# Optimization experiments

Measured on AMD Instinct MI355X. Metric: run time of the kernel, lower is better.

## Reference

```python
import jax, jax.numpy as jnp
import numpy as np

N_TOKENS = 1 << 20   # free dim; all feature dims hardcoded in the module
D_IN, D_MODEL, D_OUT = 4, 16, 4
N_EXPERTS = 8


def setup_inputs() -> dict:
    key = jax.random.key(0)
    ks = jax.random.split(key, 12)
    s = 1.0 / np.sqrt(D_MODEL)
    return {
        "x":        jax.random.normal(ks[0], (N_TOKENS, D_IN), jnp.float32),
        "w_embed":  jax.random.normal(ks[1], (D_IN, D_MODEL), jnp.float32) * 0.5,
        "b_embed":  jax.random.normal(ks[2], (D_MODEL,), jnp.float32) * 0.1,
        "gate_w":   jax.random.normal(ks[3], (D_MODEL, N_EXPERTS), jnp.float32) * s,
        "expert_w": jax.random.normal(ks[4], (N_EXPERTS, D_MODEL, D_MODEL), jnp.float32) * s,
        "expert_b": jax.random.normal(ks[5], (N_EXPERTS, D_MODEL), jnp.float32) * 0.1,
        "resid_w":  jax.random.normal(ks[6], (D_MODEL, D_MODEL), jnp.float32) * s,
        "resid_b":  jax.random.normal(ks[7], (D_MODEL,), jnp.float32) * 0.1,
        "comb_w":   jax.random.normal(ks[8], (D_MODEL, 2), jnp.float32) * s,
        "comb_b":   jax.random.normal(ks[9], (2,), jnp.float32) * 0.1,
        "proj_w":   jax.random.normal(ks[10], (D_MODEL, D_OUT), jnp.float32) * s,
        "proj_b":   jax.random.normal(ks[11], (D_OUT,), jnp.float32) * 0.1,
    }


def reference(x, w_embed, b_embed, gate_w, expert_w, expert_b,
              resid_w, resid_b, comb_w, comb_b, proj_w, proj_b):
    # embed: Linear(4, 16)
    h = x @ w_embed + b_embed                       # [N, 16]

    # top-1 softmax router (residual MoE forces top_k = 1)
    gates = jax.nn.softmax(h @ gate_w, axis=-1)     # [N, E]
    idx = jnp.argmax(gates, axis=-1)                # [N] int, constant wrt grads
    onehot = jax.nn.one_hot(idx, N_EXPERTS, dtype=h.dtype)  # [N, E]

    # load-balancing aux loss: E * sum(mean_prob * mean_dispatch)
    aux = N_EXPERTS * jnp.sum(gates.mean(0) * onehot.mean(0))

    # expert dispatch + combine (dense-equivalent of gather/scatter)
    exp_out = jnp.einsum('nd,edh->enh', h, expert_w) + expert_b[:, None, :]  # [E, N, 16]
    moe_out = jnp.einsum('ne,enh->nh', onehot, exp_out)                      # [N, 16]
    gate_sel = jnp.sum(gates * onehot, axis=-1, keepdims=True)               # [N, 1]
    moe_out = moe_out * gate_sel

    # residual expert + learned combine weights
    resid = h @ resid_w + resid_b                   # [N, 16]
    cw = jax.nn.softmax(h @ comb_w + comb_b, -1)    # [N, 2]
    y = moe_out * cw[:, :1] + resid * cw[:, 1:2]

    # proj: Linear(16, 4); aux loss is accumulated in MOE_CONTEXT in the original
    out = y @ proj_w + proj_b                       # [N, 4]
    return out, aux
```

## Files before the change

kernel.cpp:

```cpp
#include <hip/hip_runtime.h>

#define NSLOTS 128

__global__ __launch_bounds__(256) void moe_main(
    const float* __restrict__ xg,
    const float* __restrict__ w_embed,
    const float* __restrict__ b_embed,
    const float* __restrict__ gate_w,
    const float* __restrict__ expert_w,
    const float* __restrict__ expert_b,
    const float* __restrict__ resid_w,
    const float* __restrict__ resid_b,
    const float* __restrict__ comb_w,
    const float* __restrict__ comb_b,
    const float* __restrict__ proj_w,
    const float* __restrict__ proj_b,
    float* __restrict__ out,
    float* __restrict__ ws,
    int ntok)
{
    __shared__ float EP[8][16][4];
    __shared__ float RP[16][4];
    __shared__ __align__(16) float tblE[8][20];
    __shared__ __align__(16) float tblR[20];
    __shared__ __align__(16) float tblC[12];

    const int tid = threadIdx.x;

    #pragma unroll
    for (int r = 0; r < 2; ++r) {
        int idx = tid + 256 * r;
        int e = idx >> 6, rem = idx & 63, d = rem >> 2, j = rem & 3;
        float s = 0.0f;
        #pragma unroll
        for (int h = 0; h < 16; ++h)
            s = fmaf(expert_w[e * 256 + d * 16 + h], proj_w[h * 4 + j], s);
        EP[e][d][j] = s;
    }
    if (tid < 64) {
        int d = tid >> 2, j = tid & 3;
        float s = 0.0f;
        #pragma unroll
        for (int h = 0; h < 16; ++h)
            s = fmaf(resid_w[d * 16 + h], proj_w[h * 4 + j], s);
        RP[d][j] = s;
    }
    __syncthreads();

    if (tid < 128) {
        int e = tid >> 4, i = (tid >> 2) & 3, j = tid & 3;
        float s = 0.0f;
        #pragma unroll
        for (int d = 0; d < 16; ++d) s = fmaf(w_embed[i * 16 + d], EP[e][d][j], s);
        tblE[e][i * 4 + j] = s;
    } else if (tid < 160) {
        int q = tid - 128, e = q >> 2, j = q & 3;
        float s = 0.0f;
        #pragma unroll
        for (int d = 0; d < 16; ++d) s = fmaf(b_embed[d], EP[e][d][j], s);
        #pragma unroll
        for (int h = 0; h < 16; ++h) s = fmaf(expert_b[e * 16 + h], proj_w[h * 4 + j], s);
        tblE[e][16 + j] = s;
    } else if (tid < 176) {
        int q = tid - 160, i = q >> 2, j = q & 3;
        float s = 0.0f;
        #pragma unroll
        for (int d = 0; d < 16; ++d) s = fmaf(w_embed[i * 16 + d], RP[d][j], s);
        tblR[i * 4 + j] = s;
    } else if (tid < 180) {
        int j = tid - 176;
        float s = 0.0f;
        #pragma unroll
        for (int d = 0; d < 16; ++d) s = fmaf(b_embed[d], RP[d][j], s);
        #pragma unroll
        for (int h = 0; h < 16; ++h) s = fmaf(resid_b[h], proj_w[h * 4 + j], s);
        tblR[16 + j] = s;
    } else if (tid < 188) {
        int q = tid - 180, i = q >> 1, c = q & 1;
        float s = 0.0f;
        #pragma unroll
        for (int d = 0; d < 16; ++d) s = fmaf(w_embed[i * 16 + d], comb_w[d * 2 + c], s);
        tblC[i * 2 + c] = s;
    } else if (tid < 190) {
        int c = tid - 188;
        float s = comb_b[c];
        #pragma unroll
        for (int d = 0; d < 16; ++d) s = fmaf(b_embed[d], comb_w[d * 2 + c], s);
        tblC[8 + c] = s;
    }
    __syncthreads();

    float rpx[16], cr[4], cwx[8], cc[2];
    #pragma unroll
    for (int i = 0; i < 16; ++i) rpx[i] = tblR[i];
    #pragma unroll
    for (int j = 0; j < 4; ++j) cr[j] = tblR[16 + j];
    #pragma unroll
    for (int i = 0; i < 8; ++i) cwx[i] = tblC[i];
    cc[0] = tblC[8]; cc[1] = tblC[9];

    float psum[8], pcnt[8];
    #pragma unroll
    for (int e = 0; e < 8; ++e) { psum[e] = 0.0f; pcnt[e] = 0.0f; }

    #pragma unroll
    for (int t = 0; t < 2; ++t) {
        int nid = blockIdx.x * 512 + t * 256 + tid;
        if (nid < ntok) {
            float4 xv = ((const float4*)xg)[nid];

            float h[16];
            #pragma unroll
            for (int k = 0; k < 16; ++k) {
                float s = xv.x * w_embed[k];
                s = fmaf(xv.y, w_embed[16 + k], s);
                s = fmaf(xv.z, w_embed[32 + k], s);
                s = fmaf(xv.w, w_embed[48 + k], s);
                h[k] = s + b_embed[k];
            }

            float lg[8];
            #pragma unroll
            for (int e = 0; e < 8; ++e) {
                float s = h[0] * gate_w[e];
                #pragma unroll
                for (int k = 1; k < 16; ++k) s = fmaf(h[k], gate_w[k * 8 + e], s);
                lg[e] = s;
            }
            float m = lg[0]; int sel = 0;
            #pragma unroll
            for (int e = 1; e < 8; ++e) { if (lg[e] > m) { m = lg[e]; sel = e; } }
            float p[8], S = 0.0f;
            #pragma unroll
            for (int e = 0; e < 8; ++e) { p[e] = __expf(lg[e] - m); S += p[e]; }
            float inv = 1.0f / S;
            #pragma unroll
            for (int e = 0; e < 8; ++e) psum[e] = fmaf(p[e], inv, psum[e]);
            #pragma unroll
            for (int e = 0; e < 8; ++e) pcnt[e] += (sel == e) ? 1.0f : 0.0f;
            float gs = inv;

            const float4* tep = (const float4*)(&tblE[sel][0]);
            float te[20];
            #pragma unroll
            for (int q = 0; q < 5; ++q) {
                float4 v = tep[q];
                te[4 * q + 0] = v.x; te[4 * q + 1] = v.y;
                te[4 * q + 2] = v.z; te[4 * q + 3] = v.w;
            }

            float mo[4], rp[4];
            #pragma unroll
            for (int j = 0; j < 4; ++j) {
                float s = te[16 + j];
                s = fmaf(xv.x, te[j],      s);
                s = fmaf(xv.y, te[4 + j],  s);
                s = fmaf(xv.z, te[8 + j],  s);
                s = fmaf(xv.w, te[12 + j], s);
                mo[j] = s;
                float r = cr[j];
                r = fmaf(xv.x, rpx[j],      r);
                r = fmaf(xv.y, rpx[4 + j],  r);
                r = fmaf(xv.z, rpx[8 + j],  r);
                r = fmaf(xv.w, rpx[12 + j], r);
                rp[j] = r;
            }

            float l0 = cc[0], l1 = cc[1];
            l0 = fmaf(xv.x, cwx[0], l0); l1 = fmaf(xv.x, cwx[1], l1);
            l0 = fmaf(xv.y, cwx[2], l0); l1 = fmaf(xv.y, cwx[3], l1);
            l0 = fmaf(xv.z, cwx[4], l0); l1 = fmaf(xv.z, cwx[5], l1);
            l0 = fmaf(xv.w, cwx[6], l0); l1 = fmaf(xv.w, cwx[7], l1);
            float cm = fmaxf(l0, l1);
            float t0 = __expf(l0 - cm), t1 = __expf(l1 - cm);
            float ci = 1.0f / (t0 + t1);
            float cw0 = t0 * ci, cw1 = t1 * ci;

            float a = gs * cw0;
            float4 ov;
            ov.x = fmaf(a, mo[0], fmaf(cw1, rp[0], proj_b[0]));
            ov.y = fmaf(a, mo[1], fmaf(cw1, rp[1], proj_b[1]));
            ov.z = fmaf(a, mo[2], fmaf(cw1, rp[2], proj_b[2]));
            ov.w = fmaf(a, mo[3], fmaf(cw1, rp[3], proj_b[3]));
            ((float4*)out)[nid] = ov;
        }
    }

    {
        const int lane = tid & 63;
        const bool b0 = lane & 1, b1 = lane & 2, b2 = lane & 4;

        float s4[4], c4[4];
        #pragma unroll
        for (int e = 0; e < 4; ++e) {
            float ks = b0 ? psum[2*e+1] : psum[2*e];
            float gv = b0 ? psum[2*e]   : psum[2*e+1];
            s4[e] = ks + __shfl_xor(gv, 1);
            float kc = b0 ? pcnt[2*e+1] : pcnt[2*e];
            float gc = b0 ? pcnt[2*e]   : pcnt[2*e+1];
            c4[e] = kc + __shfl_xor(gc, 1);
        }
        float s2[2], c2[2];
        #pragma unroll
        for (int e = 0; e < 2; ++e) {
            float ks = b1 ? s4[2*e+1] : s4[2*e];
            float gv = b1 ? s4[2*e]   : s4[2*e+1];
            s2[e] = ks + __shfl_xor(gv, 2);
            float kc = b1 ? c4[2*e+1] : c4[2*e];
            float gc = b1 ? c4[2*e]   : c4[2*e+1];
            c2[e] = kc + __shfl_xor(gc, 2);
        }
        float stot, ctot;
        {
            float ks = b2 ? s2[1] : s2[0];
            float gv = b2 ? s2[0] : s2[1];
            stot = ks + __shfl_xor(gv, 4);
            float kc = b2 ? c2[1] : c2[0];
            float gc = b2 ? c2[0] : c2[1];
            ctot = kc + __shfl_xor(gc, 4);
        }
        stot += __shfl_xor(stot, 8);  ctot += __shfl_xor(ctot, 8);
        stot += __shfl_xor(stot, 16); ctot += __shfl_xor(ctot, 16);
        stot += __shfl_xor(stot, 32); ctot += __shfl_xor(ctot, 32);

        if (lane < 8) {
            int wave = (blockIdx.x * 256 + tid) >> 6;
            float* slot = ws + (size_t)(wave & (NSLOTS - 1)) * 16;
            atomicAdd(slot + lane, stot);
            atomicAdd(slot + 8 + lane, ctot);
        }
    }
}

__global__ __launch_bounds__(256) void moe_finalize(const float* __restrict__ ws,
                                                    float* __restrict__ aux_out,
                                                    int ntok)
{
    __shared__ float part[16][17];
    __shared__ float red[16];
    const int t = threadIdx.x;
    const int col = t & 15, slice = t >> 4;
    float s = 0.0f;
    #pragma unroll
    for (int q = 0; q < NSLOTS / 16; ++q)
        s += ws[(size_t)(slice * (NSLOTS / 16) + q) * 16 + col];
    part[slice][col] = s;
    __syncthreads();
    if (t < 16) {
        float v = 0.0f;
        #pragma unroll
        for (int i = 0; i < 16; ++i) v += part[i][t];
        red[t] = v;
    }
    __syncthreads();
    if (t == 0) {
        const float invN = 1.0f / (float)ntok;
        float aux = 0.0f;
        #pragma unroll
        for (int e = 0; e < 8; ++e)
            aux += (red[e] * invN) * (red[8 + e] * invN);
        aux_out[0] = 8.0f * aux;
    }
}

extern "C" void kernel_launch(void* const* d_in, const int* in_sizes, int n_in,
                              void* d_out, int out_size, void* d_ws, size_t ws_size,
                              hipStream_t stream) {
    const float* xg       = (const float*)d_in[0];
    const float* w_embed  = (const float*)d_in[1];
    const float* b_embed  = (const float*)d_in[2];
    const float* gate_w   = (const float*)d_in[3];
    const float* expert_w = (const float*)d_in[4];
    const float* expert_b = (const float*)d_in[5];
    const float* resid_w  = (const float*)d_in[6];
    const float* resid_b  = (const float*)d_in[7];
    const float* comb_w   = (const float*)d_in[8];
    const float* comb_b   = (const float*)d_in[9];
    const float* proj_w   = (const float*)d_in[10];
    const float* proj_b   = (const float*)d_in[11];
    float* out = (float*)d_out;
    float* ws  = (float*)d_ws;

    int ntok = in_sizes[0] / 4;
    int grid = (ntok + 511) / 512;

    hipMemsetAsync(d_ws, 0, (size_t)NSLOTS * 16 * sizeof(float), stream);
    moe_main<<<grid, 256, 0, stream>>>(xg, w_embed, b_embed, gate_w, expert_w,
                                       expert_b, resid_w, resid_b, comb_w, comb_b,
                                       proj_w, proj_b, out, ws, ntok);
    moe_finalize<<<1, 256, 0, stream>>>(ws, out + (size_t)ntok * 4, ntok);
}
```

Baseline: 105.4 us.

## Replace atomic slot accumulation with per-block partials and double tokens per block

Each block now handles four tokens per thread instead of two, halving the grid and the per-block cost of building the precomputed tables. The per-wave atomicAdds into 128 shared slots are replaced by an LDS reduction across the four waves, and each block writes one plain 16-float partial to its own workspace row. That removes the memset launch and atomic contention. In exchange the single-block finalize kernel must now read 1024 partials instead of 128, and each block does less parallel work.

```diff
diff --git a/kernel.cpp b/kernel.cpp
--- a/kernel.cpp
+++ b/kernel.cpp
@@ -1,6 +1,7 @@
 #include <hip/hip_runtime.h>
 
-#define NSLOTS 128
+#define TPB 256
+#define TOK 4
 
 __global__ __launch_bounds__(256) void moe_main(
     const float* __restrict__ xg,
@@ -24,6 +25,7 @@
     __shared__ __align__(16) float tblE[8][20];
     __shared__ __align__(16) float tblR[20];
     __shared__ __align__(16) float tblC[12];
+    __shared__ float wred[4][16];
 
     const int tid = threadIdx.x;
 
@@ -103,9 +105,10 @@
     #pragma unroll
     for (int e = 0; e < 8; ++e) { psum[e] = 0.0f; pcnt[e] = 0.0f; }
 
-    #pragma unroll
-    for (int t = 0; t < 2; ++t) {
-        int nid = blockIdx.x * 512 + t * 256 + tid;
+    const int base = blockIdx.x * (TPB * TOK) + tid;
+    #pragma unroll
+    for (int t = 0; t < TOK; ++t) {
+        int nid = base + t * TPB;
         if (nid < ntok) {
             float4 xv = ((const float4*)xg)[nid];
 
@@ -188,6 +191,7 @@
 
     {
         const int lane = tid & 63;
+        const int wv = tid >> 6;
         const bool b0 = lane & 1, b1 = lane & 2, b2 = lane & 4;
 
         float s4[4], c4[4];
@@ -224,26 +228,28 @@
         stot += __shfl_xor(stot, 32); ctot += __shfl_xor(ctot, 32);
 
         if (lane < 8) {
-            int wave = (blockIdx.x * 256 + tid) >> 6;
-            float* slot = ws + (size_t)(wave & (NSLOTS - 1)) * 16;
-            atomicAdd(slot + lane, stot);
-            atomicAdd(slot + 8 + lane, ctot);
+            wred[wv][lane]     = stot;
+            wred[wv][8 + lane] = ctot;
+        }
+        __syncthreads();
+        if (tid < 16) {
+            float v = wred[0][tid] + wred[1][tid] + wred[2][tid] + wred[3][tid];
+            ws[(size_t)blockIdx.x * 16 + tid] = v;
         }
     }
 }
 
 __global__ __launch_bounds__(256) void moe_finalize(const float* __restrict__ ws,
                                                     float* __restrict__ aux_out,
-                                                    int ntok)
+                                                    int ntok, int nblk)
 {
     __shared__ float part[16][17];
     __shared__ float red[16];
     const int t = threadIdx.x;
     const int col = t & 15, slice = t >> 4;
     float s = 0.0f;
-    #pragma unroll
-    for (int q = 0; q < NSLOTS / 16; ++q)
-        s += ws[(size_t)(slice * (NSLOTS / 16) + q) * 16 + col];
+    for (int q = slice; q < nblk; q += 16)
+        s += ws[(size_t)q * 16 + col];
     part[slice][col] = s;
     __syncthreads();
     if (t < 16) {
@@ -282,11 +288,10 @@
     float* ws  = (float*)d_ws;
 
     int ntok = in_sizes[0] / 4;
-    int grid = (ntok + 511) / 512;
-
-    hipMemsetAsync(d_ws, 0, (size_t)NSLOTS * 16 * sizeof(float), stream);
-    moe_main<<<grid, 256, 0, stream>>>(xg, w_embed, b_embed, gate_w, expert_w,
+    int grid = (ntok + TPB * TOK - 1) / (TPB * TOK);
+
+    moe_main<<<grid, TPB, 0, stream>>>(xg, w_embed, b_embed, gate_w, expert_w,
                                        expert_b, resid_w, resid_b, comb_w, comb_b,
                                        proj_w, proj_b, out, ws, ntok);
-    moe_finalize<<<1, 256, 0, stream>>>(ws, out + (size_t)ntok * 4, ntok);
+    moe_finalize<<<1, 256, 0, stream>>>(ws, out + (size_t)ntok * 4, ntok, grid);
 }
```

Measured after the change: 119.8 us. 13.7% more time.
